# Kernel optimization log

Hardware: AMD Instinct MI355X
Metric: run time of the kernel (lower is better)

## Reference

```python
import jax, jax.numpy as jnp
import numpy as np

DIM = 2048
KV_DIM = 1024
NUM_HEADS = 16
HEAD_DIM = DIM // NUM_HEADS  # 128
EPS = 1e-6
B, LQ, LKV = 2, 4096, 1024


def _rope_cos_sin(L, d, base=10000.0):
    inv_freq = 1.0 / (base ** (np.arange(0, d, 2, dtype=np.float32) / d))  # [d/2]
    freqs = np.arange(L, dtype=np.float32)[:, None] * inv_freq[None, :]   # [L, d/2]
    emb = np.concatenate([freqs, freqs], axis=-1)                          # [L, d]
    return jnp.asarray(np.cos(emb)), jnp.asarray(np.sin(emb))


def setup_inputs() -> dict:
    key = jax.random.key(0)
    ks = jax.random.split(key, 10)
    x = jax.random.normal(ks[0], (B, LQ, DIM), dtype=jnp.float32)
    y = jax.random.normal(ks[1], (B, LKV, KV_DIM), dtype=jnp.float32)
    xc, xs = _rope_cos_sin(LQ, HEAD_DIM)
    yc, ys = _rope_cos_sin(LKV, HEAD_DIM)
    x_cos = jnp.broadcast_to(xc[None], (B, LQ, HEAD_DIM))
    x_sin = jnp.broadcast_to(xs[None], (B, LQ, HEAD_DIM))
    y_cos = jnp.broadcast_to(yc[None], (B, LKV, HEAD_DIM))
    y_sin = jnp.broadcast_to(ys[None], (B, LKV, HEAD_DIM))
    s = 0.02
    Wq = jax.random.normal(ks[2], (DIM, DIM), dtype=jnp.float32) * s
    Wk = jax.random.normal(ks[3], (DIM, KV_DIM), dtype=jnp.float32) * s
    Wv = jax.random.normal(ks[4], (DIM, KV_DIM), dtype=jnp.float32) * s
    Wo = jax.random.normal(ks[5], (DIM, DIM), dtype=jnp.float32) * s
    bq = jnp.zeros((DIM,), jnp.float32)
    bk = jnp.zeros((DIM,), jnp.float32)
    bv = jnp.zeros((DIM,), jnp.float32)
    bo = jnp.zeros((DIM,), jnp.float32)
    rmsq_w = jnp.ones((DIM,), jnp.float32)
    rmsk_w = jnp.ones((DIM,), jnp.float32)
    ln_w = jnp.ones((KV_DIM,), jnp.float32)
    ln_b = jnp.zeros((KV_DIM,), jnp.float32)
    return dict(x=x, y=y, x_cos=x_cos, x_sin=x_sin, y_cos=y_cos, y_sin=y_sin,
                Wq=Wq, bq=bq, Wk=Wk, bk=bk, Wv=Wv, bv=bv, Wo=Wo, bo=bo,
                rmsq_w=rmsq_w, rmsk_w=rmsk_w, ln_w=ln_w, ln_b=ln_b)


def _rms_norm(t, w, eps=EPS):
    return t * jax.lax.rsqrt(jnp.mean(t * t, axis=-1, keepdims=True) + eps) * w


def _layer_norm(t, w, b, eps=EPS):
    mu = jnp.mean(t, axis=-1, keepdims=True)
    var = jnp.mean(jnp.square(t - mu), axis=-1, keepdims=True)
    return (t - mu) * jax.lax.rsqrt(var + eps) * w + b


def _rotate_half(t):
    d2 = t.shape[-1] // 2
    return jnp.concatenate([-t[..., d2:], t[..., :d2]], axis=-1)


def _apply_rope(t, cos, sin):
    # t: [B, L, H, D]; cos/sin: [B, L, D] -> unsqueeze head dim (unsqueeze_dim=2)
    cos = cos[:, :, None, :]
    sin = sin[:, :, None, :]
    return t * cos + _rotate_half(t) * sin


def _block_forward(x, y, x_cos, x_sin, y_cos, y_sin,
                   Wq, bq, Wk, bk, Wv, bv, Wo, bo,
                   rmsq_w, rmsk_w, ln_w, ln_b):
    Bb, Lq, D = x.shape
    Lk = y.shape[1]
    H, Dh = NUM_HEADS, HEAD_DIM
    # y pre-norm (block-level LayerNorm)
    yn = _layer_norm(y, ln_w, ln_b)
    # projections + RMSNorm on q/k
    q = _rms_norm(x @ Wq.T + bq, rmsq_w)   # [B, Lq, D]
    k = _rms_norm(yn @ Wk.T + bk, rmsk_w)  # [B, Lk, D]
    v = yn @ Wv.T + bv                     # [B, Lk, D]
    # split heads and apply RoPE
    q = _apply_rope(q.reshape(Bb, Lq, H, Dh), x_cos, x_sin)
    k = _apply_rope(k.reshape(Bb, Lk, H, Dh), y_cos, y_sin)
    v = v.reshape(Bb, Lk, H, Dh)
    # non-causal cross attention, scale = 1/sqrt(head_dim)
    scale = 1.0 / jnp.sqrt(jnp.asarray(Dh, q.dtype))
    scores = jnp.einsum('blhd,bmhd->bhlm', q, k) * scale
    probs = jax.nn.softmax(scores, axis=-1)
    out = jnp.einsum('bhlm,bmhd->blhd', probs, v).reshape(Bb, Lq, D)
    return out @ Wo.T + bo


def reference(x, y, x_cos, x_sin, y_cos, y_sin,
              Wq, bq, Wk, bk, Wv, bv, Wo, bo,
              rmsq_w, rmsk_w, ln_w, ln_b):
    return _block_forward(x, y, x_cos, x_sin, y_cos, y_sin,
                          Wq, bq, Wk, bk, Wv, bv, Wo, bo,
                          rmsq_w, rmsk_w, ln_w, ln_b)
```

## Files before the change

### kernel.cpp

```cpp
#include <hip/hip_runtime.h>


typedef __attribute__((ext_vector_type(8))) short    short8;
typedef __attribute__((ext_vector_type(8))) unsigned short ushort8;
typedef __attribute__((ext_vector_type(4))) unsigned short ushort4v;
typedef __attribute__((ext_vector_type(4))) float    f32x4;
typedef __attribute__((ext_vector_type(16))) float   f32x16;
typedef __attribute__((ext_vector_type(4))) unsigned int uint4v;

#define DEV __device__ __forceinline__

DEV unsigned short f2bf(float f) {
  unsigned int u = __builtin_bit_cast(unsigned int, f);
  u += 0x7FFFu + ((u >> 16) & 1u);
  return (unsigned short)(u >> 16);
}
DEV float bf2f(unsigned short h) {
  return __builtin_bit_cast(float, ((unsigned int)h) << 16);
}
DEV unsigned int cvtpk_bf16(float lo, float hi) {
  unsigned int r;
  asm("v_cvt_pk_bf16_f32 %0, %1, %2" : "=v"(r) : "v"(lo), "v"(hi));
  return r;
}
DEV short8 mk8(unsigned a, unsigned b, unsigned c, unsigned d) {
  uint4v t; t.x = a; t.y = b; t.z = c; t.w = d;
  return __builtin_bit_cast(short8, t);
}

DEV void gload_lds16(const void* g, void* l) {
  __builtin_amdgcn_global_load_lds(
      (const __attribute__((address_space(1))) void*)g,
      (__attribute__((address_space(3))) void*)l, 16, 0, 0);
}

__global__ __launch_bounds__(256) void cvt_kernel(const float* __restrict__ in,
                                                  unsigned short* __restrict__ out,
                                                  int n4) {
  int idx = blockIdx.x * 256 + threadIdx.x;
  int stride = gridDim.x * 256;
  for (int i = idx; i < n4; i += stride) {
    float4 v = *(const float4*)(in + (size_t)i * 4);
    ushort4v o;
    o.x = f2bf(v.x); o.y = f2bf(v.y); o.z = f2bf(v.z); o.w = f2bf(v.w);
    *(ushort4v*)(out + (size_t)i * 4) = o;
  }
}

__global__ __launch_bounds__(256) void cvt4_kernel(const float* __restrict__ s0,
                                                   const float* __restrict__ s1,
                                                   const float* __restrict__ s2,
                                                   const float* __restrict__ s3,
                                                   unsigned short* __restrict__ d0,
                                                   unsigned short* __restrict__ d1,
                                                   unsigned short* __restrict__ d2,
                                                   unsigned short* __restrict__ d3,
                                                   int n0, int n1, int n2, int n3) {
  const int total = n0 + n1 + n2 + n3;
  int idx = blockIdx.x * 256 + threadIdx.x;
  const int stride = gridDim.x * 256;
  for (int i = idx; i < total; i += stride) {
    int j = i;
    const float* s; unsigned short* d;
    if (j < n0) { s = s0; d = d0; }
    else if ((j -= n0) < n1) { s = s1; d = d1; }
    else if ((j -= n1) < n2) { s = s2; d = d2; }
    else { j -= n2; s = s3; d = d3; }
    float4 v = *(const float4*)(s + (size_t)j * 4);
    ushort4v o;
    o.x = f2bf(v.x); o.y = f2bf(v.y); o.z = f2bf(v.z); o.w = f2bf(v.w);
    *(ushort4v*)(d + (size_t)j * 4) = o;
  }
}

__global__ __launch_bounds__(256) void ln_kernel(const float* __restrict__ y,
                                                 const float* __restrict__ w,
                                                 const float* __restrict__ b,
                                                 unsigned short* __restrict__ yn) {
  const int row = blockIdx.x;
  const int t = threadIdx.x;
  const float* yr = y + (size_t)row * 1024;
  float4 v = *(const float4*)(yr + t * 4);
  float s1 = v.x + v.y + v.z + v.w;
  float s2 = v.x * v.x + v.y * v.y + v.z * v.z + v.w * v.w;
#pragma unroll
  for (int m = 1; m < 64; m <<= 1) {
    s1 += __shfl_xor(s1, m);
    s2 += __shfl_xor(s2, m);
  }
  __shared__ float red[8];
  const int wave = t >> 6, lane = t & 63;
  if (lane == 0) { red[wave] = s1; red[4 + wave] = s2; }
  __syncthreads();
  s1 = red[0] + red[1] + red[2] + red[3];
  s2 = red[4] + red[5] + red[6] + red[7];
  const float mu = s1 * (1.0f / 1024.0f);
  const float var = s2 * (1.0f / 1024.0f) - mu * mu;
  const float rs = rsqrtf(var + 1e-6f);
  ushort4v o;
  o.x = f2bf((v.x - mu) * rs * w[t * 4 + 0] + b[t * 4 + 0]);
  o.y = f2bf((v.y - mu) * rs * w[t * 4 + 1] + b[t * 4 + 1]);
  o.z = f2bf((v.z - mu) * rs * w[t * 4 + 2] + b[t * 4 + 2]);
  o.w = f2bf((v.w - mu) * rs * w[t * 4 + 3] + b[t * 4 + 3]);
  *(ushort4v*)(yn + (size_t)row * 1024 + t * 4) = o;
}

template <int EPI>
__global__ __launch_bounds__(512, 2) void gemm256(const unsigned short* __restrict__ A,
                                                  const unsigned short* __restrict__ W,
                                                  const float* __restrict__ bias0,
                                                  const float* __restrict__ bias1,
                                                  int nsplit,
                                                  void* __restrict__ Cout,
                                                  int M, int N, int K) {
  __shared__ __align__(16) char lds[2][4][16384];
  const int tid = threadIdx.x;
  const int wave = tid >> 6, lane = tid & 63;
  const int lg = lane >> 4, l15 = lane & 15;
  const int wm = wave >> 2, wn = wave & 3;

  const int nwg = gridDim.x;
  const int wgid = (blockIdx.x & 7) * (nwg >> 3) + (blockIdx.x >> 3);
  const int nbn = N >> 8;
  const int m0 = (wgid / nbn) * 256;
  const int n0 = (wgid % nbn) * 256;

  const char* Ab = (const char*)A;
  const char* Wb = (const char*)W;
  const size_t ld = (size_t)K * 2;
  const int NT = K >> 6;
  const int NI = NT >> 1;

  const int prow = tid >> 3;
  const int psw  = ((tid * 16) & 127) ^ ((prow & 7) << 4);
  const int pdst = tid * 16;
  const char* pAg = Ab + (size_t)(m0 + prow) * ld + psw;
  const char* pBg = Wb + (size_t)(n0 + prow) * ld + psw;

  f32x4 acc[8][4] = {};
  short8 af[4][2];
  short8 bf[4][2];

#define STG(BUF, HALF, ISB, TAU) do {                                         \
    const char* _g = ((ISB) ? pBg : pAg) + (size_t)(HALF) * 128 * ld +        \
                     (size_t)(TAU) * 128;                                     \
    char* _l = lds[BUF][(ISB) * 2 + (HALF)];                                  \
    gload_lds16(_g, _l + pdst);                                               \
    gload_lds16(_g + 64 * ld, _l + pdst + 8192);                              \
  } while (0)

#define LDA(BUF, H) do {                                                      \
    const char* _b = lds[BUF][wm];                                            \
    _Pragma("unroll") for (int mfl = 0; mfl < 4; ++mfl) {                     \
      const int _r = (H) * 64 + mfl * 16 + l15;                               \
      _Pragma("unroll") for (int ks = 0; ks < 2; ++ks)                        \
        af[mfl][ks] = *(const short8*)(_b + _r * 128 +                        \
                        ((ks * 64 + lg * 16) ^ ((_r & 7) << 4)));             \
    }                                                                         \
  } while (0)

#define LDB(BUF, G) do {                                                      \
    const char* _b = lds[BUF][2 + (wn >> 1)];                                 \
    _Pragma("unroll") for (int nfl = 0; nfl < 2; ++nfl) {                     \
      const int _r = (wn & 1) * 64 + (G) * 32 + nfl * 16 + l15;               \
      _Pragma("unroll") for (int ks = 0; ks < 2; ++ks)                        \
        bf[(G) * 2 + nfl][ks] = *(const short8*)(_b + _r * 128 +              \
                        ((ks * 64 + lg * 16) ^ ((_r & 7) << 4)));             \
    }                                                                         \
  } while (0)

#define MFMA_Q(H, G) do {                                                     \
    __builtin_amdgcn_s_setprio(1);                                            \
    _Pragma("unroll") for (int ks = 0; ks < 2; ++ks)                          \
    _Pragma("unroll") for (int mfl = 0; mfl < 4; ++mfl)                       \
    _Pragma("unroll") for (int nfl = 0; nfl < 2; ++nfl)                       \
      acc[(H) * 4 + mfl][(G) * 2 + nfl] =                                     \
        __builtin_amdgcn_mfma_f32_16x16x32_bf16(af[mfl][ks],                  \
            bf[(G) * 2 + nfl][ks], acc[(H) * 4 + mfl][(G) * 2 + nfl], 0,0,0); \
    __builtin_amdgcn_s_setprio(0);                                            \
  } while (0)

#define BAR() __builtin_amdgcn_s_barrier()
#define LGKM0() do { asm volatile("s_waitcnt lgkmcnt(0)" ::: "memory");       \
    __builtin_amdgcn_sched_barrier(0); } while (0)
#define VM4() asm volatile("s_waitcnt vmcnt(4)" ::: "memory")
#define VM0() asm volatile("s_waitcnt vmcnt(0)" ::: "memory")

  STG(0, 0, 0, 0); STG(0, 1, 0, 0); STG(0, 0, 1, 0); STG(0, 1, 1, 0);
  STG(1, 0, 1, 1); STG(1, 1, 1, 1);
  VM4(); BAR();

  for (int t = 0; t < NI - 1; ++t) {
    const int t2 = 2 * t;
    LDA(0, 0); LDB(0, 0); STG(1, 0, 0, t2 + 1);
    BAR(); LGKM0(); MFMA_Q(0, 0); BAR();
    LDB(0, 1); STG(1, 1, 0, t2 + 1);
    BAR(); LGKM0(); MFMA_Q(0, 1); BAR();
    LDA(0, 1); STG(0, 0, 1, t2 + 2);
    BAR(); LGKM0(); MFMA_Q(1, 1); BAR();
    STG(0, 1, 1, t2 + 2);
    BAR(); MFMA_Q(1, 0); VM4(); BAR();
    LDA(1, 0); LDB(1, 0); STG(0, 0, 0, t2 + 2);
    BAR(); LGKM0(); MFMA_Q(0, 0); BAR();
    LDB(1, 1); STG(0, 1, 0, t2 + 2);
    BAR(); LGKM0(); MFMA_Q(0, 1); BAR();
    LDA(1, 1); STG(1, 0, 1, t2 + 3);
    BAR(); LGKM0(); MFMA_Q(1, 1); BAR();
    STG(1, 1, 1, t2 + 3);
    BAR(); MFMA_Q(1, 0); VM4(); BAR();
  }

  LDA(0, 0); LDB(0, 0); STG(1, 0, 0, NT - 1);
  BAR(); LGKM0(); MFMA_Q(0, 0); BAR();
  LDB(0, 1); STG(1, 1, 0, NT - 1);
  BAR(); LGKM0(); MFMA_Q(0, 1); BAR();
  LDA(0, 1);
  BAR(); LGKM0(); MFMA_Q(1, 1); BAR();
  BAR(); MFMA_Q(1, 0); VM0(); BAR();
  LDA(1, 0); LDB(1, 0); LGKM0(); MFMA_Q(0, 0);
  LDB(1, 1); LGKM0(); MFMA_Q(0, 1);
  LDA(1, 1); LGKM0(); MFMA_Q(1, 1);
  MFMA_Q(1, 0);

#undef STG
#undef LDA
#undef LDB
#undef MFMA_Q
#undef BAR
#undef LGKM0
#undef VM4
#undef VM0

#pragma unroll
  for (int nf = 0; nf < 4; ++nf) {
    const int n = n0 + wn * 64 + nf * 16 + l15;
    const float bv = (n < nsplit) ? bias0[n] : bias1[n - nsplit];
#pragma unroll
    for (int mf = 0; mf < 8; ++mf) {
      const int mB = m0 + wm * 128 + mf * 16 + lg * 4;
#pragma unroll
      for (int r = 0; r < 4; ++r) {
        const float v = acc[mf][nf][r] + bv;
        if constexpr (EPI == 0)
          ((unsigned short*)Cout)[(size_t)(mB + r) * N + n] = f2bf(v);
        else
          ((float*)Cout)[(size_t)(mB + r) * N + n] = v;
      }
    }
  }
}

__global__ __launch_bounds__(256) void rmsrope_kernel(const unsigned short* __restrict__ in,
                                                      const float* __restrict__ w,
                                                      const float* __restrict__ cs,
                                                      const float* __restrict__ sn,
                                                      unsigned short* __restrict__ out,
                                                      int L, int ldin, float scale) {
  const int row = blockIdx.x;
  const int t = threadIdx.x;
  __shared__ __align__(16) unsigned short srow[2048];
  __shared__ float red[4];
  const unsigned short* ir = in + (size_t)row * ldin;
  ushort8 v = *(const ushort8*)(ir + t * 8);
  float vals[8];
  float ss = 0.f;
#pragma unroll
  for (int j = 0; j < 8; ++j) { vals[j] = bf2f(v[j]); ss += vals[j] * vals[j]; }
  *(ushort8*)(srow + t * 8) = v;
#pragma unroll
  for (int m = 1; m < 64; m <<= 1) ss += __shfl_xor(ss, m);
  const int wave = t >> 6, lane = t & 63;
  if (lane == 0) red[wave] = ss;
  __syncthreads();
  const float tot = red[0] + red[1] + red[2] + red[3];
  const float rms = rsqrtf(tot * (1.0f / 2048.0f) + 1e-6f);

  const int n0 = t * 8;
  const int d0 = n0 & 127;
  const int hh = n0 >> 7;
  const float sign = (d0 < 64) ? -1.0f : 1.0f;
  const float* cb = cs + (size_t)row * 128 + d0;
  const float* sb = sn + (size_t)row * 128 + d0;
  ushort8 po = *(const ushort8*)(srow + (n0 ^ 64));
  ushort8 ou;
#pragma unroll
  for (int j = 0; j < 8; ++j) {
    const float self = vals[j] * rms * w[n0 + j];
    const float part = bf2f(po[j]) * rms * w[(n0 ^ 64) + j];
    ou[j] = f2bf((self * cb[j] + sign * part * sb[j]) * scale);
  }
  const int b = row / L, l = row - (row / L) * L;
  *(ushort8*)(out + (((size_t)(b * 16 + hh)) * L + l) * 128 + d0) = ou;
}

__global__ __launch_bounds__(256) void vtrans_kernel(const unsigned short* __restrict__ vpre,
                                                     unsigned short* __restrict__ vt,
                                                     int ldv) {
  const int bid = blockIdx.x;
  const int kt = bid & 15, bh = bid >> 4;
  const int h = bh & 15, b = bh >> 4;
  __shared__ unsigned short lt[64][130];
  const int t = threadIdx.x;
  const int i0 = t >> 4, c0 = (t & 15) * 8;
  const unsigned short* src = vpre + ((size_t)(b * 1024 + kt * 64)) * ldv + h * 128;
#pragma unroll
  for (int ii = 0; ii < 4; ++ii) {
    const int i = i0 + ii * 16;
    ushort8 v = *(const ushort8*)(src + (size_t)i * ldv + c0);
#pragma unroll
    for (int j = 0; j < 8; ++j) lt[i][c0 + j] = v[j];
  }
  __syncthreads();
  const int d0 = t >> 3, j0 = (t & 7) * 8;
  unsigned short* dst = vt + (size_t)bh * 128 * 1024 + kt * 64;
#pragma unroll
  for (int dd = 0; dd < 4; ++dd) {
    const int d = d0 + dd * 32;
    ushort8 o;
#pragma unroll
    for (int jj = 0; jj < 8; ++jj) o[jj] = lt[j0 + jj][d];
    *(ushort8*)(dst + (size_t)d * 1024 + j0) = o;
  }
}

__global__ __launch_bounds__(512, 2) void attn_kernel(const unsigned short* __restrict__ q,
                                                      const unsigned short* __restrict__ k,
                                                      const unsigned short* __restrict__ vt,
                                                      unsigned short* __restrict__ ao) {
  __shared__ __align__(16) char sK[2][2][64 * 256];
  __shared__ __align__(16) char sV[2][2][64 * 256];

  const int bid0 = blockIdx.x;
  const int bid = (bid0 & 7) * 64 + (bid0 >> 3);
  const int qt = bid & 15, bh = bid >> 4;
  const int tid = threadIdx.x;
  const int wave = tid >> 6, lane = tid & 63;
  const int l31 = lane & 31, hi = lane >> 5;
  const bool hib = (hi != 0);

  const unsigned short* qbase = q + (((size_t)bh * 4096) + qt * 256 + wave * 32) * 128;
  const char* kbase = (const char*)(k + (size_t)bh * 1024 * 128);
  const char* vbase = (const char*)(vt + (size_t)bh * 128 * 1024);

  short8 qb[8];
#pragma unroll
  for (int step = 0; step < 8; ++step)
    qb[step] = *(const short8*)(qbase + (size_t)l31 * 128 + step * 16 + hi * 8);

  f32x16 o[4] = {};
  float lsum = 0.f;

#define STAGE_KV(BUF, KV0) do {                                              \
    _Pragma("unroll")                                                        \
    for (int sub = 0; sub < 2; ++sub) {                                      \
      _Pragma("unroll")                                                      \
      for (int i = 0; i < 2; ++i) {                                          \
        const int p = (i * 512 + tid) * 16;                                  \
        const int row = p >> 8;                                              \
        const int si = (p & 255) ^ ((row & 15) << 4);                        \
        gload_lds16(kbase + (size_t)((KV0) + sub * 64 + row) * 256 + si,     \
                    sK[BUF][sub] + p);                                       \
      }                                                                      \
      _Pragma("unroll")                                                      \
      for (int i = 0; i < 2; ++i) {                                          \
        const int p = (i * 512 + tid) * 16;                                  \
        const int row = p >> 8;                                              \
        const int si = (p & 255) ^ ((row & 15) << 4);                        \
        const int d = 2 * row + (si >> 7);                                   \
        gload_lds16(vbase + (size_t)d * 2048 + ((KV0) + sub * 64) * 2 +      \
                    (si & 127), sV[BUF][sub] + p);                           \
      }                                                                      \
    }                                                                        \
  } while (0)

#define QK(K, S0, S1) do {                                                   \
    const int ksw = (l31 & 15) << 4;                                         \
    _Pragma("unroll") for (int step = 0; step < 8; ++step) {                 \
      const int cb2 = step * 32 + hi * 16;                                   \
      short8 kf0 = *(const short8*)((K) + l31 * 256 + (cb2 ^ ksw));          \
      short8 kf1 = *(const short8*)((K) + (32 + l31) * 256 + (cb2 ^ ksw));   \
      S0 = __builtin_amdgcn_mfma_f32_32x32x16_bf16(kf0, qb[step], S0, 0,0,0);\
      S1 = __builtin_amdgcn_mfma_f32_32x32x16_bf16(kf1, qb[step], S1, 0,0,0);\
    }                                                                        \
  } while (0)

#define SOFTMAX_PV(V, SS, F) do {                                            \
    float p_[16];                                                            \
    _Pragma("unroll") for (int r = 0; r < 16; ++r) p_[r] = exp2f((SS)[r]);   \
    lsum += (((p_[0]+p_[1])+(p_[2]+p_[3])) + ((p_[4]+p_[5])+(p_[6]+p_[7])))  \
          + (((p_[8]+p_[9])+(p_[10]+p_[11])) + ((p_[12]+p_[13])+(p_[14]+p_[15])));\
    const unsigned w0 = cvtpk_bf16(p_[0], p_[1]),  w1 = cvtpk_bf16(p_[2], p_[3]), \
                   w2 = cvtpk_bf16(p_[4], p_[5]),  w3 = cvtpk_bf16(p_[6], p_[7]), \
                   w4 = cvtpk_bf16(p_[8], p_[9]),  w5 = cvtpk_bf16(p_[10], p_[11]),\
                   w6 = cvtpk_bf16(p_[12], p_[13]),w7 = cvtpk_bf16(p_[14], p_[15]);\
    const unsigned x0 = (unsigned)__shfl_xor((int)(hib ? w0 : w2), 32);      \
    const unsigned x1 = (unsigned)__shfl_xor((int)(hib ? w1 : w3), 32);      \
    const unsigned x2 = (unsigned)__shfl_xor((int)(hib ? w4 : w6), 32);      \
    const unsigned x3 = (unsigned)__shfl_xor((int)(hib ? w5 : w7), 32);      \
    const short8 fr0 = mk8(hib ? x0 : w0, hib ? x1 : w1,                     \
                           hib ? w2 : x0, hib ? w3 : x1);                    \
    const short8 fr1 = mk8(hib ? x2 : w4, hib ? x3 : w5,                     \
                           hib ? w6 : x2, hib ? w7 : x3);                    \
    _Pragma("unroll") for (int kstep = 0; kstep < 2; ++kstep) {              \
      const short8 pa = kstep ? fr1 : fr0;                                   \
      const int colb = (F) * 64 + kstep * 32 + hi * 16;                      \
      _Pragma("unroll") for (int dt = 0; dt < 4; ++dt) {                     \
        const int vrow = dt * 16 + (l31 >> 1);                               \
        const int inner = (l31 & 1) * 128 + colb;                            \
        short8 vf = *(const short8*)((V) + vrow * 256 +                      \
                                     (inner ^ ((vrow & 15) << 4)));          \
        o[dt] = __builtin_amdgcn_mfma_f32_32x32x16_bf16(pa, vf, o[dt], 0,0,0);\
      }                                                                      \
    }                                                                        \
  } while (0)

#define TILE(BUF) do {                                                       \
    f32x16 s0 = {}, s1 = {}, s2 = {}, s3 = {};                               \
    QK(sK[BUF][0], s0, s1);                                                  \
    QK(sK[BUF][1], s2, s3);                                                  \
    SOFTMAX_PV(sV[BUF][0], s0, 0);                                           \
    SOFTMAX_PV(sV[BUF][0], s1, 1);                                           \
    SOFTMAX_PV(sV[BUF][1], s2, 0);                                           \
    SOFTMAX_PV(sV[BUF][1], s3, 1);                                           \
  } while (0)

  STAGE_KV(0, 0);
  __syncthreads();

#pragma unroll 1
  for (int kt2 = 0; kt2 < 4; ++kt2) {
    STAGE_KV(1, (2 * kt2 + 1) * 128);
    TILE(0);
    __syncthreads();
    if (kt2 < 3) STAGE_KV(0, (2 * kt2 + 2) * 128);
    TILE(1);
    __syncthreads();
  }
#undef STAGE_KV
#undef QK
#undef SOFTMAX_PV
#undef TILE

  lsum += __shfl_xor(lsum, 32);
  const float linv = 1.0f / lsum;
  const int b = bh >> 4, h = bh & 15;
#pragma unroll
  for (int r = 0; r < 16; ++r) {
    const int crow = (r & 3) + 8 * (r >> 2) + 4 * hi;
    const float inv = __shfl(linv, crow);
    const int qg = qt * 256 + wave * 32 + crow;
    const size_t orow = ((size_t)b * 4096 + qg) * 2048 + h * 128;
#pragma unroll
    for (int dt = 0; dt < 4; ++dt)
      ao[orow + dt * 32 + l31] = f2bf(o[dt][r] * inv);
  }
}

extern "C" void kernel_launch(void* const* d_in, const int* in_sizes, int n_in,
                              void* d_out, int out_size, void* d_ws, size_t ws_size,
                              hipStream_t stream) {
  (void)in_sizes; (void)n_in; (void)out_size; (void)ws_size;
  const float* x      = (const float*)d_in[0];
  const float* y      = (const float*)d_in[1];
  const float* x_cos  = (const float*)d_in[2];
  const float* x_sin  = (const float*)d_in[3];
  const float* y_cos  = (const float*)d_in[4];
  const float* y_sin  = (const float*)d_in[5];
  const float* Wq     = (const float*)d_in[6];
  const float* bq     = (const float*)d_in[7];
  const float* Wk     = (const float*)d_in[8];
  const float* bk     = (const float*)d_in[9];
  const float* Wv     = (const float*)d_in[10];
  const float* bv     = (const float*)d_in[11];
  const float* Wo     = (const float*)d_in[12];
  const float* bo     = (const float*)d_in[13];
  const float* rmsq_w = (const float*)d_in[14];
  const float* rmsk_w = (const float*)d_in[15];
  const float* ln_w   = (const float*)d_in[16];
  const float* ln_b   = (const float*)d_in[17];

  char* ws = (char*)d_ws;
  unsigned short* xb    = (unsigned short*)(ws + 0);
  unsigned short* Wqb   = (unsigned short*)(ws + 33554432);
  unsigned short* Wkb   = (unsigned short*)(ws + 41943040);
  unsigned short* Wvb   = (unsigned short*)(ws + 46137344);
  unsigned short* Wob   = (unsigned short*)(ws + 50331648);
  unsigned short* ynb   = (unsigned short*)(ws + 58720256);
  unsigned short* kvpre = (unsigned short*)(ws + 62914560);
  unsigned short* qpre  = (unsigned short*)(ws + 62914560);
  unsigned short* qr    = (unsigned short*)(ws + 96468992);
  unsigned short* kr    = (unsigned short*)(ws + 130023424);
  unsigned short* vt    = (unsigned short*)(ws + 138412032);
  unsigned short* ao    = xb;

  const float qscale = 1.4426950408889634f * 0.08838834764831843f;

  cvt_kernel<<<2048, 256, 0, stream>>>(x, xb, (2 * 4096 * 2048) / 4);
  cvt4_kernel<<<2048, 256, 0, stream>>>(Wq, Wk, Wv, Wo, Wqb, Wkb, Wvb, Wob,
                                        (2048 * 2048) / 4, (2048 * 1024) / 4,
                                        (2048 * 1024) / 4, (2048 * 2048) / 4);
  ln_kernel<<<2048, 256, 0, stream>>>(y, ln_w, ln_b, ynb);

  gemm256<0><<<128, 512, 0, stream>>>(ynb, Wkb, bk, bv, 2048, kvpre, 2048, 4096, 1024);
  rmsrope_kernel<<<2048, 256, 0, stream>>>(kvpre, rmsk_w, y_cos, y_sin, kr, 1024, 4096, 1.0f);
  vtrans_kernel<<<512, 256, 0, stream>>>(kvpre + 2048, vt, 4096);

  gemm256<0><<<256, 512, 0, stream>>>(xb, Wqb, bq, bq, 2048, qpre, 8192, 2048, 2048);
  rmsrope_kernel<<<8192, 256, 0, stream>>>(qpre, rmsq_w, x_cos, x_sin, qr, 4096, 2048, qscale);

  attn_kernel<<<512, 512, 0, stream>>>(qr, kr, vt, ao);

  gemm256<1><<<256, 512, 0, stream>>>(ao, Wob, bo, bo, 2048, (float*)d_out, 8192, 2048, 2048);
}
```

Baseline: 313.1 us.

## Merge prep, projection GEMMs and post-processing into fewer combined launches

```diff
diff --git a/kernel.cpp b/kernel.cpp
--- a/kernel.cpp
+++ b/kernel.cpp
@@ -34,38 +34,61 @@
       (__attribute__((address_space(3))) void*)l, 16, 0, 0);
 }
 
-__global__ __launch_bounds__(256) void cvt_kernel(const float* __restrict__ in,
-                                                  unsigned short* __restrict__ out,
-                                                  int n4) {
-  int idx = blockIdx.x * 256 + threadIdx.x;
-  int stride = gridDim.x * 256;
-  for (int i = idx; i < n4; i += stride) {
-    float4 v = *(const float4*)(in + (size_t)i * 4);
+__global__ __launch_bounds__(256) void prep_kernel(const float* __restrict__ y,
+                                                   const float* __restrict__ lnw,
+                                                   const float* __restrict__ lnb,
+                                                   unsigned short* __restrict__ yn,
+                                                   const float* __restrict__ x,
+                                                   const float* __restrict__ Wq,
+                                                   const float* __restrict__ Wk,
+                                                   const float* __restrict__ Wv,
+                                                   const float* __restrict__ Wo,
+                                                   unsigned short* __restrict__ xb,
+                                                   unsigned short* __restrict__ Wqb,
+                                                   unsigned short* __restrict__ Wkb,
+                                                   unsigned short* __restrict__ Wvb,
+                                                   unsigned short* __restrict__ Wob) {
+  const int t = threadIdx.x;
+  if (blockIdx.x < 2048) {
+    const int row = blockIdx.x;
+    const float* yr = y + (size_t)row * 1024;
+    float4 v = *(const float4*)(yr + t * 4);
+    float s1 = v.x + v.y + v.z + v.w;
+    float s2 = v.x * v.x + v.y * v.y + v.z * v.z + v.w * v.w;
+#pragma unroll
+    for (int m = 1; m < 64; m <<= 1) {
+      s1 += __shfl_xor(s1, m);
+      s2 += __shfl_xor(s2, m);
+    }
+    __shared__ float red[8];
+    const int wave = t >> 6, lane = t & 63;
+    if (lane == 0) { red[wave] = s1; red[4 + wave] = s2; }
+    __syncthreads();
+    s1 = red[0] + red[1] + red[2] + red[3];
+    s2 = red[4] + red[5] + red[6] + red[7];
+    const float mu = s1 * (1.0f / 1024.0f);
+    const float var = s2 * (1.0f / 1024.0f) - mu * mu;
+    const float rs = rsqrtf(var + 1e-6f);
     ushort4v o;
-    o.x = f2bf(v.x); o.y = f2bf(v.y); o.z = f2bf(v.z); o.w = f2bf(v.w);
-    *(ushort4v*)(out + (size_t)i * 4) = o;
-  }
-}
-
-__global__ __launch_bounds__(256) void cvt4_kernel(const float* __restrict__ s0,
-                                                   const float* __restrict__ s1,
-                                                   const float* __restrict__ s2,
-                                                   const float* __restrict__ s3,
-                                                   unsigned short* __restrict__ d0,
-                                                   unsigned short* __restrict__ d1,
-                                                   unsigned short* __restrict__ d2,
-                                                   unsigned short* __restrict__ d3,
-                                                   int n0, int n1, int n2, int n3) {
-  const int total = n0 + n1 + n2 + n3;
-  int idx = blockIdx.x * 256 + threadIdx.x;
-  const int stride = gridDim.x * 256;
-  for (int i = idx; i < total; i += stride) {
+    o.x = f2bf((v.x - mu) * rs * lnw[t * 4 + 0] + lnb[t * 4 + 0]);
+    o.y = f2bf((v.y - mu) * rs * lnw[t * 4 + 1] + lnb[t * 4 + 1]);
+    o.z = f2bf((v.z - mu) * rs * lnw[t * 4 + 2] + lnb[t * 4 + 2]);
+    o.w = f2bf((v.w - mu) * rs * lnw[t * 4 + 3] + lnb[t * 4 + 3]);
+    *(ushort4v*)(yn + (size_t)row * 1024 + t * 4) = o;
+    return;
+  }
+  const int nx = 4194304, nwq = 1048576, nwk = 524288, nwv = 524288;
+  const int total = 7340032;
+  int i = (blockIdx.x - 2048) * 256 + t;
+  const int stride = 1536 * 256;
+  for (; i < total; i += stride) {
     int j = i;
     const float* s; unsigned short* d;
-    if (j < n0) { s = s0; d = d0; }
-    else if ((j -= n0) < n1) { s = s1; d = d1; }
-    else if ((j -= n1) < n2) { s = s2; d = d2; }
-    else { j -= n2; s = s3; d = d3; }
+    if (j < nx) { s = x; d = xb; }
+    else if ((j -= nx) < nwq) { s = Wq; d = Wqb; }
+    else if ((j -= nwq) < nwk) { s = Wk; d = Wkb; }
+    else if ((j -= nwk) < nwv) { s = Wv; d = Wvb; }
+    else { j -= nwv; s = Wo; d = Wob; }
     float4 v = *(const float4*)(s + (size_t)j * 4);
     ushort4v o;
     o.x = f2bf(v.x); o.y = f2bf(v.y); o.z = f2bf(v.z); o.w = f2bf(v.w);
@@ -73,54 +96,19 @@
   }
 }
 
-__global__ __launch_bounds__(256) void ln_kernel(const float* __restrict__ y,
-                                                 const float* __restrict__ w,
-                                                 const float* __restrict__ b,
-                                                 unsigned short* __restrict__ yn) {
-  const int row = blockIdx.x;
-  const int t = threadIdx.x;
-  const float* yr = y + (size_t)row * 1024;
-  float4 v = *(const float4*)(yr + t * 4);
-  float s1 = v.x + v.y + v.z + v.w;
-  float s2 = v.x * v.x + v.y * v.y + v.z * v.z + v.w * v.w;
-#pragma unroll
-  for (int m = 1; m < 64; m <<= 1) {
-    s1 += __shfl_xor(s1, m);
-    s2 += __shfl_xor(s2, m);
-  }
-  __shared__ float red[8];
-  const int wave = t >> 6, lane = t & 63;
-  if (lane == 0) { red[wave] = s1; red[4 + wave] = s2; }
-  __syncthreads();
-  s1 = red[0] + red[1] + red[2] + red[3];
-  s2 = red[4] + red[5] + red[6] + red[7];
-  const float mu = s1 * (1.0f / 1024.0f);
-  const float var = s2 * (1.0f / 1024.0f) - mu * mu;
-  const float rs = rsqrtf(var + 1e-6f);
-  ushort4v o;
-  o.x = f2bf((v.x - mu) * rs * w[t * 4 + 0] + b[t * 4 + 0]);
-  o.y = f2bf((v.y - mu) * rs * w[t * 4 + 1] + b[t * 4 + 1]);
-  o.z = f2bf((v.z - mu) * rs * w[t * 4 + 2] + b[t * 4 + 2]);
-  o.w = f2bf((v.w - mu) * rs * w[t * 4 + 3] + b[t * 4 + 3]);
-  *(ushort4v*)(yn + (size_t)row * 1024 + t * 4) = o;
-}
-
 template <int EPI>
-__global__ __launch_bounds__(512, 2) void gemm256(const unsigned short* __restrict__ A,
-                                                  const unsigned short* __restrict__ W,
-                                                  const float* __restrict__ bias0,
-                                                  const float* __restrict__ bias1,
-                                                  int nsplit,
-                                                  void* __restrict__ Cout,
-                                                  int M, int N, int K) {
-  __shared__ __align__(16) char lds[2][4][16384];
-  const int tid = threadIdx.x;
+DEV void gemm256_body(const unsigned short* __restrict__ A,
+                      const unsigned short* __restrict__ W,
+                      const float* __restrict__ bias0,
+                      const float* __restrict__ bias1,
+                      int nsplit, void* __restrict__ Cout,
+                      int M, int N, int K,
+                      int bidLocal, int nwg, char* ldsb, int tid) {
   const int wave = tid >> 6, lane = tid & 63;
   const int lg = lane >> 4, l15 = lane & 15;
   const int wm = wave >> 2, wn = wave & 3;
 
-  const int nwg = gridDim.x;
-  const int wgid = (blockIdx.x & 7) * (nwg >> 3) + (blockIdx.x >> 3);
+  const int wgid = (bidLocal & 7) * (nwg >> 3) + (bidLocal >> 3);
   const int nbn = N >> 8;
   const int m0 = (wgid / nbn) * 256;
   const int n0 = (wgid % nbn) * 256;
@@ -141,16 +129,18 @@
   short8 af[4][2];
   short8 bf[4][2];
 
+#define LDSB(BUF, SEG) (ldsb + ((BUF) * 4 + (SEG)) * 16384)
+
 #define STG(BUF, HALF, ISB, TAU) do {                                         \
     const char* _g = ((ISB) ? pBg : pAg) + (size_t)(HALF) * 128 * ld +        \
                      (size_t)(TAU) * 128;                                     \
-    char* _l = lds[BUF][(ISB) * 2 + (HALF)];                                  \
+    char* _l = LDSB(BUF, (ISB) * 2 + (HALF));                                 \
     gload_lds16(_g, _l + pdst);                                               \
     gload_lds16(_g + 64 * ld, _l + pdst + 8192);                              \
   } while (0)
 
 #define LDA(BUF, H) do {                                                      \
-    const char* _b = lds[BUF][wm];                                            \
+    const char* _b = LDSB(BUF, wm);                                           \
     _Pragma("unroll") for (int mfl = 0; mfl < 4; ++mfl) {                     \
       const int _r = (H) * 64 + mfl * 16 + l15;                               \
       _Pragma("unroll") for (int ks = 0; ks < 2; ++ks)                        \
@@ -160,7 +150,7 @@
   } while (0)
 
 #define LDB(BUF, G) do {                                                      \
-    const char* _b = lds[BUF][2 + (wn >> 1)];                                 \
+    const char* _b = LDSB(BUF, 2 + (wn >> 1));                                \
     _Pragma("unroll") for (int nfl = 0; nfl < 2; ++nfl) {                     \
       const int _r = (wn & 1) * 64 + (G) * 32 + nfl * 16 + l15;               \
       _Pragma("unroll") for (int ks = 0; ks < 2; ++ks)                        \
@@ -230,6 +220,7 @@
 #undef LGKM0
 #undef VM4
 #undef VM0
+#undef LDSB
 
 #pragma unroll
   for (int nf = 0; nf < 4; ++nf) {
@@ -250,16 +241,42 @@
   }
 }
 
-__global__ __launch_bounds__(256) void rmsrope_kernel(const unsigned short* __restrict__ in,
-                                                      const float* __restrict__ w,
-                                                      const float* __restrict__ cs,
-                                                      const float* __restrict__ sn,
-                                                      unsigned short* __restrict__ out,
-                                                      int L, int ldin, float scale) {
-  const int row = blockIdx.x;
+__global__ __launch_bounds__(512, 2) void gemm_dual(const unsigned short* __restrict__ xb,
+                                                    const unsigned short* __restrict__ Wqb,
+                                                    const float* __restrict__ bq,
+                                                    unsigned short* __restrict__ qpre,
+                                                    const unsigned short* __restrict__ ynb,
+                                                    const unsigned short* __restrict__ Wkb,
+                                                    const float* __restrict__ bk,
+                                                    const float* __restrict__ bv,
+                                                    unsigned short* __restrict__ kvpre) {
+  __shared__ __align__(16) char lds[2][4][16384];
+  if (blockIdx.x < 256)
+    gemm256_body<0>(xb, Wqb, bq, bq, 2048, qpre, 8192, 2048, 2048,
+                    blockIdx.x, 256, &lds[0][0][0], threadIdx.x);
+  else
+    gemm256_body<0>(ynb, Wkb, bk, bv, 2048, kvpre, 2048, 4096, 1024,
+                    blockIdx.x - 256, 128, &lds[0][0][0], threadIdx.x);
+}
+
+__global__ __launch_bounds__(512, 2) void gemm_f32(const unsigned short* __restrict__ A,
+                                                   const unsigned short* __restrict__ W,
+                                                   const float* __restrict__ bias,
+                                                   float* __restrict__ C,
+                                                   int M, int N, int K) {
+  __shared__ __align__(16) char lds[2][4][16384];
+  gemm256_body<1>(A, W, bias, bias, N, C, M, N, K,
+                  blockIdx.x, 256, &lds[0][0][0], threadIdx.x);
+}
+
+DEV void rmsrope_body(const unsigned short* __restrict__ in,
+                      const float* __restrict__ w,
+                      const float* __restrict__ cs,
+                      const float* __restrict__ sn,
+                      unsigned short* __restrict__ out,
+                      int L, int ldin, float scale, int row,
+                      unsigned short* srow, float* red) {
   const int t = threadIdx.x;
-  __shared__ __align__(16) unsigned short srow[2048];
-  __shared__ float red[4];
   const unsigned short* ir = in + (size_t)row * ldin;
   ushort8 v = *(const ushort8*)(ir + t * 8);
   float vals[8];
@@ -293,13 +310,11 @@
   *(ushort8*)(out + (((size_t)(b * 16 + hh)) * L + l) * 128 + d0) = ou;
 }
 
-__global__ __launch_bounds__(256) void vtrans_kernel(const unsigned short* __restrict__ vpre,
-                                                     unsigned short* __restrict__ vt,
-                                                     int ldv) {
-  const int bid = blockIdx.x;
+DEV void vtrans_body(const unsigned short* __restrict__ vpre,
+                     unsigned short* __restrict__ vt, int ldv, int bid,
+                     unsigned short (*lt)[130]) {
   const int kt = bid & 15, bh = bid >> 4;
   const int h = bh & 15, b = bh >> 4;
-  __shared__ unsigned short lt[64][130];
   const int t = threadIdx.x;
   const int i0 = t >> 4, c0 = (t & 15) * 8;
   const unsigned short* src = vpre + ((size_t)(b * 1024 + kt * 64)) * ldv + h * 128;
@@ -320,6 +335,31 @@
 #pragma unroll
     for (int jj = 0; jj < 8; ++jj) o[jj] = lt[j0 + jj][d];
     *(ushort8*)(dst + (size_t)d * 1024 + j0) = o;
+  }
+}
+
+__global__ __launch_bounds__(256) void post_kernel(const unsigned short* __restrict__ qpre,
+                                                   const float* __restrict__ rmsq_w,
+                                                   const float* __restrict__ x_cos,
+                                                   const float* __restrict__ x_sin,
+                                                   unsigned short* __restrict__ qr,
+                                                   const unsigned short* __restrict__ kvpre,
+                                                   const float* __restrict__ rmsk_w,
+                                                   const float* __restrict__ y_cos,
+                                                   const float* __restrict__ y_sin,
+                                                   unsigned short* __restrict__ kr,
+                                                   unsigned short* __restrict__ vt,
+                                                   float qscale) {
+  __shared__ __align__(16) unsigned short srow[2048];
+  __shared__ float red[4];
+  __shared__ unsigned short lt[64][130];
+  const int b = blockIdx.x;
+  if (b < 8192) {
+    rmsrope_body(qpre, rmsq_w, x_cos, x_sin, qr, 4096, 2048, qscale, b, srow, red);
+  } else if (b < 10240) {
+    rmsrope_body(kvpre, rmsk_w, y_cos, y_sin, kr, 1024, 4096, 1.0f, b - 8192, srow, red);
+  } else {
+    vtrans_body(kvpre + 2048, vt, 4096, b - 10240, lt);
   }
 }
 
@@ -486,29 +526,21 @@
   unsigned short* Wvb   = (unsigned short*)(ws + 46137344);
   unsigned short* Wob   = (unsigned short*)(ws + 50331648);
   unsigned short* ynb   = (unsigned short*)(ws + 58720256);
-  unsigned short* kvpre = (unsigned short*)(ws + 62914560);
   unsigned short* qpre  = (unsigned short*)(ws + 62914560);
-  unsigned short* qr    = (unsigned short*)(ws + 96468992);
-  unsigned short* kr    = (unsigned short*)(ws + 130023424);
-  unsigned short* vt    = (unsigned short*)(ws + 138412032);
+  unsigned short* kvpre = (unsigned short*)(ws + 96468992);
+  unsigned short* qr    = (unsigned short*)(ws + 113246208);
+  unsigned short* kr    = (unsigned short*)(ws + 33554432);
+  unsigned short* vt    = (unsigned short*)(ws + 41943040);
   unsigned short* ao    = xb;
+  (void)Wvb;
 
   const float qscale = 1.4426950408889634f * 0.08838834764831843f;
 
-  cvt_kernel<<<2048, 256, 0, stream>>>(x, xb, (2 * 4096 * 2048) / 4);
-  cvt4_kernel<<<2048, 256, 0, stream>>>(Wq, Wk, Wv, Wo, Wqb, Wkb, Wvb, Wob,
-                                        (2048 * 2048) / 4, (2048 * 1024) / 4,
-                                        (2048 * 1024) / 4, (2048 * 2048) / 4);
-  ln_kernel<<<2048, 256, 0, stream>>>(y, ln_w, ln_b, ynb);
-
-  gemm256<0><<<128, 512, 0, stream>>>(ynb, Wkb, bk, bv, 2048, kvpre, 2048, 4096, 1024);
-  rmsrope_kernel<<<2048, 256, 0, stream>>>(kvpre, rmsk_w, y_cos, y_sin, kr, 1024, 4096, 1.0f);
-  vtrans_kernel<<<512, 256, 0, stream>>>(kvpre + 2048, vt, 4096);
-
-  gemm256<0><<<256, 512, 0, stream>>>(xb, Wqb, bq, bq, 2048, qpre, 8192, 2048, 2048);
-  rmsrope_kernel<<<8192, 256, 0, stream>>>(qpre, rmsq_w, x_cos, x_sin, qr, 4096, 2048, qscale);
-
+  prep_kernel<<<3584, 256, 0, stream>>>(y, ln_w, ln_b, ynb, x, Wq, Wk, Wv, Wo,
+                                        xb, Wqb, Wkb, Wvb, Wob);
+  gemm_dual<<<384, 512, 0, stream>>>(xb, Wqb, bq, qpre, ynb, Wkb, bk, bv, kvpre);
+  post_kernel<<<10752, 256, 0, stream>>>(qpre, rmsq_w, x_cos, x_sin, qr,
+                                         kvpre, rmsk_w, y_cos, y_sin, kr, vt, qscale);
   attn_kernel<<<512, 512, 0, stream>>>(qr, kr, vt, ao);
-
-  gemm256<1><<<256, 512, 0, stream>>>(ao, Wob, bo, bo, 2048, (float*)d_out, 8192, 2048, 2048);
-}
+  gemm_f32<<<256, 512, 0, stream>>>(ao, Wob, bo, (float*)d_out, 8192, 2048, 2048);
+}
```

Result: faster. 303.4 us (-3.1%).
